# Kernel optimization log

Measured on AMD Instinct MI355X. Metric: run time of the kernel, lower is better.

The kernel has to match this reference:

```python
import jax, jax.numpy as jnp
import numpy as np

D = 1024      # n_embd
F = 1024      # moe_inter_dim (ffn_hidden_size)
E = 8         # moe_num_experts
K = 2         # moe_top_k
B, T = 2, 2048


def setup_inputs() -> dict:
    key = jax.random.key(0)
    ks = jax.random.split(key, 7)
    std = 0.02
    x = jax.random.normal(ks[0], (B, T, D), dtype=jnp.float32)
    router_w = jax.random.normal(ks[1], (D, E), dtype=jnp.float32) * std
    w1 = jax.random.normal(ks[2], (E, D, F), dtype=jnp.float32) * std  # expert up proj
    w2 = jax.random.normal(ks[3], (E, F, D), dtype=jnp.float32) * std  # expert down proj
    shared_gate_up = jax.random.normal(ks[4], (D, 2 * F), dtype=jnp.float32) * std
    shared_down = jax.random.normal(ks[5], (F, D), dtype=jnp.float32) * std
    shared_gate_w = jax.random.normal(ks[6], (D, 1), dtype=jnp.float32) * std
    return {"x": x, "router_w": router_w, "w1": w1, "w2": w2,
            "shared_gate_up": shared_gate_up, "shared_down": shared_down,
            "shared_gate_w": shared_gate_w}


def _moe_forward(x, router_w, w1, w2, shared_gate_up, shared_down, shared_gate_w):
    b, t, d = x.shape
    xf = x.reshape(-1, d)                                   # [N, D]
    n = xf.shape[0]

    # --- router: softmax over experts, top-k scores used directly as combine weights ---
    logits = xf @ router_w                                  # [N, E]
    probs = jax.nn.softmax(logits, axis=-1)
    topw, topi = jax.lax.top_k(probs, K)                    # [N, K]
    combine = jnp.zeros((n, E), dtype=probs.dtype).at[
        jnp.arange(n)[:, None], topi].add(topw)             # [N, E] sparse combine weights

    # --- expert MLP: h = silu(x @ w1_e) @ w2_e, combined with routing weights ---
    h = jax.nn.silu(jnp.einsum('nd,edf->nef', xf, w1))      # [N, E, F]
    ye = jnp.einsum('nef,efd->ned', h, w2)                  # [N, E, D]
    routed = jnp.einsum('ne,ned->nd', combine, ye)          # [N, D]

    # --- shared expert SwiGLU, gated by sigmoid(x @ shared_gate_w) ---
    gu = xf @ shared_gate_up                                # [N, 2F]
    gate, up = gu[:, :F], gu[:, F:]
    shared = (jax.nn.silu(gate) * up) @ shared_down         # [N, D]
    shared = jax.nn.sigmoid(xf @ shared_gate_w) * shared

    return (routed + shared).reshape(b, t, d)


def reference(x, router_w, w1, w2, shared_gate_up, shared_down, shared_gate_w):
    return _moe_forward(x, router_w, w1, w2, shared_gate_up, shared_down, shared_gate_w)
```

## Files before the change

kernel.cpp:

```cpp
#include <hip/hip_runtime.h>
#include <math.h>

typedef __bf16 bf16_t;
typedef __bf16 bf16x8 __attribute__((ext_vector_type(8)));
typedef __bf16 bf16x4 __attribute__((ext_vector_type(4)));
typedef float f32x4 __attribute__((ext_vector_type(4)));

#define N_TOK 4096
#define DMODEL 1024
#define FFN 1024
#define NEXP 8
#define HIST_BLK 16

#define BM 128
#define BN 128
#define BK 32
#define LDK 32

__device__ __forceinline__ void gload16(const bf16_t* g, bf16_t* l) {
  __builtin_amdgcn_global_load_lds((const __attribute__((address_space(1))) void*)g,
                                   (__attribute__((address_space(3))) void*)l, 16, 0, 0);
}

__global__ void transpose_all_kernel(const float* __restrict__ w1, const float* __restrict__ w2,
                                     const float* __restrict__ sgu, const float* __restrict__ sdw,
                                     bf16_t* __restrict__ w1t, bf16_t* __restrict__ w2t,
                                     bf16_t* __restrict__ sgut, bf16_t* __restrict__ sdt) {
  __shared__ float tile[32][33];
  const int z = blockIdx.z;
  const float* in;
  bf16_t* out;
  int C = 1024;
  bool remap = false;
  if (z < 8) {
    in = w1 + (size_t)z * 1048576; out = w1t + (size_t)z * 1048576;
  } else if (z < 16) {
    in = w2 + (size_t)(z - 8) * 1048576; out = w2t + (size_t)(z - 8) * 1048576;
  } else if (z == 16) {
    in = sgu; out = sgut; C = 2048; remap = true;
  } else {
    in = sdw; out = sdt;
  }
  const int R = 1024;
  const int c0 = blockIdx.x * 32, r0 = blockIdx.y * 32;
  if (c0 >= C) return;
  const int tx = threadIdx.x, ty = threadIdx.y;
#pragma unroll
  for (int i = 0; i < 32; i += 8)
    tile[ty + i][tx] = in[(size_t)(r0 + ty + i) * C + (c0 + tx)];
  __syncthreads();
#pragma unroll
  for (int i = 0; i < 32; i += 8) {
    int c = c0 + ty + i;
    int oc = remap ? ((c < FFN) ? 2 * c : 2 * (c - FFN) + 1) : c;
    out[(size_t)oc * R + (r0 + tx)] = (bf16_t)tile[tx][ty + i];
  }
}

__global__ void router_kernel(const float* __restrict__ x, const float* __restrict__ rw,
                              const float* __restrict__ gw, bf16_t* __restrict__ xb,
                              int* __restrict__ topi, float* __restrict__ topw,
                              float* __restrict__ sig) {
  const int t = blockIdx.x;
  const int lane = threadIdx.x;
  const float* xr = x + (size_t)t * DMODEL;
  bf16_t* xbr = xb + (size_t)t * DMODEL;
  float acc[NEXP] = {0.f, 0.f, 0.f, 0.f, 0.f, 0.f, 0.f, 0.f};
  float accg = 0.f;
#pragma unroll
  for (int i = 0; i < 4; i++) {
    const int d = i * 256 + lane * 4;
    float4 xv = *reinterpret_cast<const float4*>(xr + d);
    bf16x4 o;
    o[0] = (bf16_t)xv.x; o[1] = (bf16_t)xv.y; o[2] = (bf16_t)xv.z; o[3] = (bf16_t)xv.w;
    *reinterpret_cast<bf16x4*>(xbr + d) = o;
    const float xs[4] = {xv.x, xv.y, xv.z, xv.w};
#pragma unroll
    for (int j = 0; j < 4; j++) {
      const float4* r = reinterpret_cast<const float4*>(rw + (size_t)(d + j) * NEXP);
      float4 r0 = r[0], r1 = r[1];
      float xj = xs[j];
      acc[0] += xj * r0.x; acc[1] += xj * r0.y; acc[2] += xj * r0.z; acc[3] += xj * r0.w;
      acc[4] += xj * r1.x; acc[5] += xj * r1.y; acc[6] += xj * r1.z; acc[7] += xj * r1.w;
      accg += xj * gw[d + j];
    }
  }
#pragma unroll
  for (int e = 0; e < NEXP; e++)
    for (int s = 32; s > 0; s >>= 1) acc[e] += __shfl_down(acc[e], s, 64);
  for (int s = 32; s > 0; s >>= 1) accg += __shfl_down(accg, s, 64);
  if (lane == 0) {
    float mx = acc[0];
#pragma unroll
    for (int e = 1; e < NEXP; e++) mx = fmaxf(mx, acc[e]);
    float p[NEXP], sum = 0.f;
#pragma unroll
    for (int e = 0; e < NEXP; e++) { p[e] = __expf(acc[e] - mx); sum += p[e]; }
    int i1 = 0;
#pragma unroll
    for (int e = 1; e < NEXP; e++) if (acc[e] > acc[i1]) i1 = e;
    int i2 = (i1 == 0) ? 1 : 0;
#pragma unroll
    for (int e = 0; e < NEXP; e++) if (e != i1 && acc[e] > acc[i2]) i2 = e;
    float inv = 1.f / sum;
    topi[2 * t] = i1;     topw[2 * t] = p[i1] * inv;
    topi[2 * t + 1] = i2; topw[2 * t + 1] = p[i2] * inv;
    sig[t] = 1.f / (1.f + __expf(-accg));
  }
}

__global__ void hist_kernel(const int* __restrict__ topi, int* __restrict__ block_counts) {
  __shared__ int h[NEXP];
  const int tid = threadIdx.x;
  if (tid < NEXP) h[tid] = 0;
  __syncthreads();
  const int t = blockIdx.x * 256 + tid;
  atomicAdd(&h[topi[2 * t]], 1);
  atomicAdd(&h[topi[2 * t + 1]], 1);
  __syncthreads();
  if (tid < NEXP) block_counts[blockIdx.x * NEXP + tid] = h[tid];
}

__global__ void gather_kernel(const int* __restrict__ topi, const float* __restrict__ topw,
                              const int* __restrict__ block_counts, int* __restrict__ slot_tok,
                              float* __restrict__ slot_w, int* __restrict__ slot_of,
                              int* __restrict__ offsets, int* __restrict__ counts) {
  __shared__ int cur[NEXP];
  const int tid = threadIdx.x;
  if (tid < NEXP) {
    int off = 0;
    for (int f = 0; f < tid; f++)
      for (int b = 0; b < HIST_BLK; b++) off += block_counts[b * NEXP + f];
    int bb = off;
    for (int b = 0; b < (int)blockIdx.x; b++) bb += block_counts[b * NEXP + tid];
    cur[tid] = bb;
    if (blockIdx.x == 0) {
      offsets[tid] = off;
      int tot = 0;
      for (int b = 0; b < HIST_BLK; b++) tot += block_counts[b * NEXP + tid];
      counts[tid] = tot;
    }
  }
  __syncthreads();
  const int t = blockIdx.x * 256 + tid;
#pragma unroll
  for (int j = 0; j < 2; j++) {
    int e = topi[2 * t + j];
    int s = atomicAdd(&cur[e], 1);
    slot_tok[s] = t;
    slot_w[s] = topw[2 * t + j];
    slot_of[2 * t + j] = s;
  }
}

__global__ void combine_kernel(const bf16_t* __restrict__ Y, const int* __restrict__ slot_of,
                               float* __restrict__ out) {
  int i = blockIdx.x * blockDim.x + threadIdx.x;
  int t = i >> 7;
  int d = (i & 127) << 3;
  int s0 = slot_of[2 * t], s1 = slot_of[2 * t + 1];
  bf16x8 a = *reinterpret_cast<const bf16x8*>(Y + (size_t)s0 * DMODEL + d);
  bf16x8 b = *reinterpret_cast<const bf16x8*>(Y + (size_t)s1 * DMODEL + d);
  float* o = out + (size_t)t * DMODEL + d;
  float4 o0 = *reinterpret_cast<float4*>(o);
  float4 o1 = *reinterpret_cast<float4*>(o + 4);
  o0.x += (float)a[0] + (float)b[0]; o0.y += (float)a[1] + (float)b[1];
  o0.z += (float)a[2] + (float)b[2]; o0.w += (float)a[3] + (float)b[3];
  o1.x += (float)a[4] + (float)b[4]; o1.y += (float)a[5] + (float)b[5];
  o1.z += (float)a[6] + (float)b[6]; o1.w += (float)a[7] + (float)b[7];
  *reinterpret_cast<float4*>(o) = o0;
  *reinterpret_cast<float4*>(o + 4) = o1;
}

template <int MODE>
__global__ __launch_bounds__(256) void gemm_kernel(
    const bf16_t* __restrict__ A, const bf16_t* __restrict__ B, void* __restrict__ Cout,
    int N, const int* __restrict__ offsets, const int* __restrict__ counts,
    const int* __restrict__ slot_tok, const float* __restrict__ slot_w,
    const float* __restrict__ sig) {
  __shared__ bf16_t lds_a[BM * LDK];
  __shared__ bf16_t lds_b[BN * LDK];

  const int e = blockIdx.z;
  int m0, mEnd;
  const bf16_t* Bp = B;
  if (MODE == 1 || MODE == 2) {
    const int off = offsets[e], cnt = counts[e];
    m0 = off + (int)blockIdx.y * BM;
    mEnd = off + cnt;
    if (m0 >= mEnd) return;
    Bp += (size_t)e * FFN * DMODEL;
  } else {
    m0 = blockIdx.y * BM;
    mEnd = N_TOK;
  }
  const int n0 = blockIdx.x * BN;

  const int tid = threadIdx.x;
  const int lane = tid & 63;
  const int wave = tid >> 6;
  const int wm = (wave >> 1) * 64;
  const int wn = (wave & 1) * 64;
  const int qd = lane >> 4;
  const int lm = lane & 15;

  const int srow = wave * 16 + (lane >> 2);
  const int chunk = (lane & 3) ^ ((lane >> 3) & 3);
  const bf16_t* pa[2];
  const bf16_t* pb[2];
#pragma unroll
  for (int h = 0; h < 2; h++) {
    int s = m0 + srow + h * 64;
    int g;
    if (MODE == 1) g = slot_tok[(s < mEnd) ? s : (mEnd - 1)];
    else if (MODE == 2) g = (s < mEnd) ? s : (mEnd - 1);
    else g = s;
    pa[h] = A + (size_t)g * 1024 + chunk * 8;
    pb[h] = Bp + (size_t)(n0 + srow + h * 64) * 1024 + chunk * 8;
  }
  bf16_t* la[2] = {&lds_a[(wave * 16) * LDK], &lds_a[(64 + wave * 16) * LDK]};
  bf16_t* lb[2] = {&lds_b[(wave * 16) * LDK], &lds_b[(64 + wave * 16) * LDK]};

  f32x4 acc[4][4] = {};

  const int rkey = (lm >> 1) & 3;

  for (int k0 = 0; k0 < 1024; k0 += BK) {
    __syncthreads();
#pragma unroll
    for (int h = 0; h < 2; h++) {
      gload16(pa[h] + k0, la[h]);
      gload16(pb[h] + k0, lb[h]);
    }
    __syncthreads();
    bf16x8 af[4], bfr[4];
#pragma unroll
    for (int i = 0; i < 4; i++)
      af[i] = *reinterpret_cast<const bf16x8*>(
          &lds_a[(wm + i * 16 + lm) * LDK + ((qd ^ rkey) * 8)]);
#pragma unroll
    for (int j = 0; j < 4; j++)
      bfr[j] = *reinterpret_cast<const bf16x8*>(
          &lds_b[(wn + j * 16 + lm) * LDK + ((qd ^ rkey) * 8)]);
#pragma unroll
    for (int i = 0; i < 4; i++)
#pragma unroll
      for (int j = 0; j < 4; j++)
        acc[i][j] = __builtin_amdgcn_mfma_f32_16x16x32_bf16(af[i], bfr[j], acc[i][j], 0, 0, 0);
  }

#pragma unroll
  for (int i = 0; i < 4; i++) {
#pragma unroll
    for (int r = 0; r < 4; r++) {
      const int gm = m0 + wm + i * 16 + qd * 4 + r;
      const bool mOk = (MODE == 0 || MODE == 3) || (gm < mEnd);
      const float wgt = (MODE == 2 && mOk) ? slot_w[gm] : 0.f;
#pragma unroll
      for (int j = 0; j < 4; j++) {
        const int col = n0 + wn + j * 16 + lm;
        float v = acc[i][j][r];
        if (MODE == 0) {
          float u = __shfl_xor(v, 1, 64);
          if ((lane & 1) == 0) {
            float sv = v / (1.f + __expf(-v)) * u;
            ((bf16_t*)Cout)[(size_t)gm * FFN + (col >> 1)] = (bf16_t)sv;
          }
        } else if (MODE == 1) {
          if (mOk) ((bf16_t*)Cout)[(size_t)gm * FFN + col] = (bf16_t)(v / (1.f + __expf(-v)));
        } else if (MODE == 2) {
          if (mOk) ((bf16_t*)Cout)[(size_t)gm * DMODEL + col] = (bf16_t)(wgt * v);
        } else {
          ((float*)Cout)[(size_t)gm * DMODEL + col] = sig[gm] * v;
        }
      }
    }
  }
}

extern "C" void kernel_launch(void* const* d_in, const int* in_sizes, int n_in, void* d_out,
                              int out_size, void* d_ws, size_t ws_size, hipStream_t stream) {
  const float* x = (const float*)d_in[0];
  const float* rw = (const float*)d_in[1];
  const float* w1 = (const float*)d_in[2];
  const float* w2 = (const float*)d_in[3];
  const float* sgu = (const float*)d_in[4];
  const float* sdw = (const float*)d_in[5];
  const float* gw = (const float*)d_in[6];
  float* out = (float*)d_out;

  char* ws = (char*)d_ws;
  size_t off = 0;
  auto alloc = [&](size_t bytes) -> void* {
    void* p = ws + off;
    off += (bytes + 255) & ~(size_t)255;
    return p;
  };
  bf16_t* xb = (bf16_t*)alloc((size_t)N_TOK * DMODEL * 2);
  bf16_t* w1t = (bf16_t*)alloc((size_t)NEXP * DMODEL * FFN * 2);
  bf16_t* w2t = (bf16_t*)alloc((size_t)NEXP * DMODEL * FFN * 2);
  bf16_t* sgut = (bf16_t*)alloc((size_t)2 * FFN * DMODEL * 2);
  bf16_t* sdt = (bf16_t*)alloc((size_t)DMODEL * FFN * 2);
  bf16_t* S = (bf16_t*)alloc((size_t)N_TOK * FFN * 2);
  bf16_t* H = (bf16_t*)alloc((size_t)N_TOK * 2 * FFN * 2);
  bf16_t* Y = (bf16_t*)alloc((size_t)N_TOK * 2 * DMODEL * 2);
  int* topi = (int*)alloc(N_TOK * 2 * 4);
  float* topw = (float*)alloc(N_TOK * 2 * 4);
  float* sig = (float*)alloc(N_TOK * 4);
  int* slot_tok = (int*)alloc(N_TOK * 2 * 4);
  float* slot_w = (float*)alloc(N_TOK * 2 * 4);
  int* slot_of = (int*)alloc(N_TOK * 2 * 4);
  int* block_counts = (int*)alloc(HIST_BLK * NEXP * 4);
  int* counts = (int*)alloc(NEXP * 4);
  int* offsets = (int*)alloc(NEXP * 4);

  transpose_all_kernel<<<dim3(64, 32, 18), dim3(32, 8), 0, stream>>>(w1, w2, sgu, sdw, w1t, w2t,
                                                                     sgut, sdt);
  router_kernel<<<N_TOK, 64, 0, stream>>>(x, rw, gw, xb, topi, topw, sig);
  hist_kernel<<<HIST_BLK, 256, 0, stream>>>(topi, block_counts);
  gather_kernel<<<HIST_BLK, 256, 0, stream>>>(topi, topw, block_counts, slot_tok, slot_w,
                                              slot_of, offsets, counts);

  gemm_kernel<0><<<dim3(2 * FFN / BN, N_TOK / BM, 1), 256, 0, stream>>>(
      xb, sgut, S, 2 * FFN, nullptr, nullptr, nullptr, nullptr, nullptr);
  gemm_kernel<1><<<dim3(FFN / BN, N_TOK / BM, NEXP), 256, 0, stream>>>(
      xb, w1t, H, FFN, offsets, counts, slot_tok, nullptr, nullptr);
  gemm_kernel<2><<<dim3(DMODEL / BN, N_TOK / BM, NEXP), 256, 0, stream>>>(
      H, w2t, Y, DMODEL, offsets, counts, slot_tok, slot_w, nullptr);
  gemm_kernel<3><<<dim3(DMODEL / BN, N_TOK / BM, 1), 256, 0, stream>>>(
      S, sdt, out, DMODEL, nullptr, nullptr, nullptr, nullptr, sig);
  combine_kernel<<<N_TOK * DMODEL / 8 / 256, 256, 0, stream>>>(Y, slot_of, out);
}
```

Measured before the change: 290.2 us.

## Merge shared and routed expert GEMMs into two combined launches

Merges the shared-expert up-projection with the routed expert up-projection into one launch, and the shared down-projection with the routed down-projection into another, using blockIdx.z to select the workload. This cuts launches from four to two and lets the shared and routed blocks fill the GPU together instead of each GEMM leaving a tail of idle compute units. In exchange, every block does extra runtime branching on the workload type, and register pressure may rise because both epilogues are compiled into one kernel.

```diff
diff --git a/kernel.cpp b/kernel.cpp
--- a/kernel.cpp
+++ b/kernel.cpp
@@ -172,29 +172,36 @@
   *reinterpret_cast<float4*>(o + 4) = o1;
 }
 
-template <int MODE>
+template <int PHASE>
 __global__ __launch_bounds__(256) void gemm_kernel(
-    const bf16_t* __restrict__ A, const bf16_t* __restrict__ B, void* __restrict__ Cout,
-    int N, const int* __restrict__ offsets, const int* __restrict__ counts,
+    const bf16_t* __restrict__ As, const bf16_t* __restrict__ Bs, void* __restrict__ Cs,
+    const bf16_t* __restrict__ Ae, const bf16_t* __restrict__ Be, void* __restrict__ Ce,
+    const int* __restrict__ offsets, const int* __restrict__ counts,
     const int* __restrict__ slot_tok, const float* __restrict__ slot_w,
     const float* __restrict__ sig) {
   __shared__ bf16_t lds_a[BM * LDK];
   __shared__ bf16_t lds_b[BN * LDK];
 
-  const int e = blockIdx.z;
-  int m0, mEnd;
-  const bf16_t* Bp = B;
-  if (MODE == 1 || MODE == 2) {
+  const int z = blockIdx.z;
+  const bool sh = (PHASE == 0) ? (z < 2) : (z == 0);
+  int m0, mEnd, n0;
+  const bf16_t* Ap;
+  const bf16_t* Bp;
+  void* Cp;
+  if (sh) {
+    n0 = (PHASE == 0) ? ((z * 8 + blockIdx.x) * BN) : (blockIdx.x * BN);
+    m0 = blockIdx.y * BM;
+    mEnd = N_TOK;
+    Ap = As; Bp = Bs; Cp = Cs;
+  } else {
+    const int e = (PHASE == 0) ? (z - 2) : (z - 1);
     const int off = offsets[e], cnt = counts[e];
     m0 = off + (int)blockIdx.y * BM;
     mEnd = off + cnt;
     if (m0 >= mEnd) return;
-    Bp += (size_t)e * FFN * DMODEL;
-  } else {
-    m0 = blockIdx.y * BM;
-    mEnd = N_TOK;
-  }
-  const int n0 = blockIdx.x * BN;
+    n0 = blockIdx.x * BN;
+    Ap = Ae; Bp = Be + (size_t)e * FFN * DMODEL; Cp = Ce;
+  }
 
   const int tid = threadIdx.x;
   const int lane = tid & 63;
@@ -211,11 +218,9 @@
 #pragma unroll
   for (int h = 0; h < 2; h++) {
     int s = m0 + srow + h * 64;
-    int g;
-    if (MODE == 1) g = slot_tok[(s < mEnd) ? s : (mEnd - 1)];
-    else if (MODE == 2) g = (s < mEnd) ? s : (mEnd - 1);
-    else g = s;
-    pa[h] = A + (size_t)g * 1024 + chunk * 8;
+    int sc = (s < mEnd) ? s : (mEnd - 1);
+    int g = (PHASE == 0 && !sh) ? slot_tok[sc] : sc;
+    pa[h] = Ap + (size_t)g * 1024 + chunk * 8;
     pb[h] = Bp + (size_t)(n0 + srow + h * 64) * 1024 + chunk * 8;
   }
   bf16_t* la[2] = {&lds_a[(wave * 16) * LDK], &lds_a[(64 + wave * 16) * LDK]};
@@ -254,24 +259,28 @@
 #pragma unroll
     for (int r = 0; r < 4; r++) {
       const int gm = m0 + wm + i * 16 + qd * 4 + r;
-      const bool mOk = (MODE == 0 || MODE == 3) || (gm < mEnd);
-      const float wgt = (MODE == 2 && mOk) ? slot_w[gm] : 0.f;
+      const bool mOk = sh || (gm < mEnd);
+      const float wgt = (PHASE == 1 && !sh && mOk) ? slot_w[gm] : 0.f;
 #pragma unroll
       for (int j = 0; j < 4; j++) {
         const int col = n0 + wn + j * 16 + lm;
         float v = acc[i][j][r];
-        if (MODE == 0) {
-          float u = __shfl_xor(v, 1, 64);
-          if ((lane & 1) == 0) {
-            float sv = v / (1.f + __expf(-v)) * u;
-            ((bf16_t*)Cout)[(size_t)gm * FFN + (col >> 1)] = (bf16_t)sv;
+        if (PHASE == 0) {
+          if (sh) {
+            float u = __shfl_xor(v, 1, 64);
+            if ((lane & 1) == 0) {
+              float sv = v / (1.f + __expf(-v)) * u;
+              ((bf16_t*)Cp)[(size_t)gm * FFN + (col >> 1)] = (bf16_t)sv;
+            }
+          } else {
+            if (mOk) ((bf16_t*)Cp)[(size_t)gm * FFN + col] = (bf16_t)(v / (1.f + __expf(-v)));
           }
-        } else if (MODE == 1) {
-          if (mOk) ((bf16_t*)Cout)[(size_t)gm * FFN + col] = (bf16_t)(v / (1.f + __expf(-v)));
-        } else if (MODE == 2) {
-          if (mOk) ((bf16_t*)Cout)[(size_t)gm * DMODEL + col] = (bf16_t)(wgt * v);
         } else {
-          ((float*)Cout)[(size_t)gm * DMODEL + col] = sig[gm] * v;
+          if (sh) {
+            ((float*)Cp)[(size_t)gm * DMODEL + col] = sig[gm] * v;
+          } else {
+            if (mOk) ((bf16_t*)Cp)[(size_t)gm * DMODEL + col] = (bf16_t)(wgt * v);
+          }
         }
       }
     }
@@ -321,13 +330,9 @@
   gather_kernel<<<HIST_BLK, 256, 0, stream>>>(topi, topw, block_counts, slot_tok, slot_w,
                                               slot_of, offsets, counts);
 
-  gemm_kernel<0><<<dim3(2 * FFN / BN, N_TOK / BM, 1), 256, 0, stream>>>(
-      xb, sgut, S, 2 * FFN, nullptr, nullptr, nullptr, nullptr, nullptr);
-  gemm_kernel<1><<<dim3(FFN / BN, N_TOK / BM, NEXP), 256, 0, stream>>>(
-      xb, w1t, H, FFN, offsets, counts, slot_tok, nullptr, nullptr);
-  gemm_kernel<2><<<dim3(DMODEL / BN, N_TOK / BM, NEXP), 256, 0, stream>>>(
-      H, w2t, Y, DMODEL, offsets, counts, slot_tok, slot_w, nullptr);
-  gemm_kernel<3><<<dim3(DMODEL / BN, N_TOK / BM, 1), 256, 0, stream>>>(
-      S, sdt, out, DMODEL, nullptr, nullptr, nullptr, nullptr, sig);
+  gemm_kernel<0><<<dim3(8, N_TOK / BM, 2 + NEXP), 256, 0, stream>>>(
+      xb, sgut, S, xb, w1t, H, offsets, counts, slot_tok, nullptr, nullptr);
+  gemm_kernel<1><<<dim3(DMODEL / BN, N_TOK / BM, 1 + NEXP), 256, 0, stream>>>(
+      S, sdt, out, H, w2t, Y, offsets, counts, slot_tok, slot_w, sig);
   combine_kernel<<<N_TOK * DMODEL / 8 / 256, 256, 0, stream>>>(Y, slot_of, out);
 }
```

Result: slower. 300.1 us (+3.4%).

## Double-buffer LDS tiles with BK=64 to overlap global loads and MFMA

Applied to the files above, without the earlier changes.

Doubles the K tile to 64 and adds a two-stage LDS ping-pong buffer, so the async global-to-LDS loads for the next tile are issued before the MFMAs on the current tile, replacing the load-sync-compute-sync pattern. The XOR swizzle is adjusted to 8 chunks per row and the staging layout changes so each wave loads 8 rows per pass. This is meant to hide global memory latency and halve barrier count. In exchange LDS usage rises to 64 KB per block, which may reduce occupancy.

```diff
diff --git a/kernel.cpp b/kernel.cpp
--- a/kernel.cpp
+++ b/kernel.cpp
@@ -14,8 +14,8 @@
 
 #define BM 128
 #define BN 128
-#define BK 32
-#define LDK 32
+#define BK 64
+#define NT (1024 / BK)
 
 __device__ __forceinline__ void gload16(const bf16_t* g, bf16_t* l) {
   __builtin_amdgcn_global_load_lds((const __attribute__((address_space(1))) void*)g,
@@ -178,8 +178,7 @@
     int N, const int* __restrict__ offsets, const int* __restrict__ counts,
     const int* __restrict__ slot_tok, const float* __restrict__ slot_w,
     const float* __restrict__ sig) {
-  __shared__ bf16_t lds_a[BM * LDK];
-  __shared__ bf16_t lds_b[BN * LDK];
+  __shared__ bf16_t lds[2][(BM + BN) * BK];
 
   const int e = blockIdx.z;
   int m0, mEnd;
@@ -204,49 +203,58 @@
   const int qd = lane >> 4;
   const int lm = lane & 15;
 
-  const int srow = wave * 16 + (lane >> 2);
-  const int chunk = (lane & 3) ^ ((lane >> 3) & 3);
-  const bf16_t* pa[2];
-  const bf16_t* pb[2];
-#pragma unroll
-  for (int h = 0; h < 2; h++) {
-    int s = m0 + srow + h * 64;
+  const int rsub = lane >> 3;
+  const int chunk = (lane & 7) ^ rsub;
+  const bf16_t* pa[4];
+  const bf16_t* pb[4];
+#pragma unroll
+  for (int h = 0; h < 4; h++) {
+    const int ar = h * 32 + wave * 8 + rsub;
+    int s = m0 + ar;
+    int sc = (s < mEnd) ? s : (mEnd - 1);
     int g;
-    if (MODE == 1) g = slot_tok[(s < mEnd) ? s : (mEnd - 1)];
-    else if (MODE == 2) g = (s < mEnd) ? s : (mEnd - 1);
+    if (MODE == 1) g = slot_tok[sc];
+    else if (MODE == 2) g = sc;
     else g = s;
     pa[h] = A + (size_t)g * 1024 + chunk * 8;
-    pb[h] = Bp + (size_t)(n0 + srow + h * 64) * 1024 + chunk * 8;
-  }
-  bf16_t* la[2] = {&lds_a[(wave * 16) * LDK], &lds_a[(64 + wave * 16) * LDK]};
-  bf16_t* lb[2] = {&lds_b[(wave * 16) * LDK], &lds_b[(64 + wave * 16) * LDK]};
+    pb[h] = Bp + (size_t)(n0 + ar) * 1024 + chunk * 8;
+  }
+
+  auto stage = [&](int bf, int k0) {
+#pragma unroll
+    for (int h = 0; h < 4; h++) {
+      gload16(pa[h] + k0, &lds[bf][(h * 32 + wave * 8) * BK]);
+      gload16(pb[h] + k0, &lds[bf][(BM + h * 32 + wave * 8) * BK]);
+    }
+  };
 
   f32x4 acc[4][4] = {};
-
-  const int rkey = (lm >> 1) & 3;
-
-  for (int k0 = 0; k0 < 1024; k0 += BK) {
+  const int pc0 = qd ^ (lm & 7);
+  const int pc1 = (4 + qd) ^ (lm & 7);
+
+  stage(0, 0);
+  __syncthreads();
+  for (int t = 0; t < NT; ++t) {
+    const int cur = t & 1;
+    if (t + 1 < NT) stage(cur ^ 1, (t + 1) * BK);
+#pragma unroll
+    for (int s = 0; s < 2; s++) {
+      const int pc = (s == 0) ? pc0 : pc1;
+      bf16x8 af[4], bfr[4];
+#pragma unroll
+      for (int i = 0; i < 4; i++)
+        af[i] = *reinterpret_cast<const bf16x8*>(&lds[cur][(wm + i * 16 + lm) * BK + pc * 8]);
+#pragma unroll
+      for (int j = 0; j < 4; j++)
+        bfr[j] =
+            *reinterpret_cast<const bf16x8*>(&lds[cur][(BM + wn + j * 16 + lm) * BK + pc * 8]);
+#pragma unroll
+      for (int i = 0; i < 4; i++)
+#pragma unroll
+        for (int j = 0; j < 4; j++)
+          acc[i][j] = __builtin_amdgcn_mfma_f32_16x16x32_bf16(af[i], bfr[j], acc[i][j], 0, 0, 0);
+    }
     __syncthreads();
-#pragma unroll
-    for (int h = 0; h < 2; h++) {
-      gload16(pa[h] + k0, la[h]);
-      gload16(pb[h] + k0, lb[h]);
-    }
-    __syncthreads();
-    bf16x8 af[4], bfr[4];
-#pragma unroll
-    for (int i = 0; i < 4; i++)
-      af[i] = *reinterpret_cast<const bf16x8*>(
-          &lds_a[(wm + i * 16 + lm) * LDK + ((qd ^ rkey) * 8)]);
-#pragma unroll
-    for (int j = 0; j < 4; j++)
-      bfr[j] = *reinterpret_cast<const bf16x8*>(
-          &lds_b[(wn + j * 16 + lm) * LDK + ((qd ^ rkey) * 8)]);
-#pragma unroll
-    for (int i = 0; i < 4; i++)
-#pragma unroll
-      for (int j = 0; j < 4; j++)
-        acc[i][j] = __builtin_amdgcn_mfma_f32_16x16x32_bf16(af[i], bfr[j], acc[i][j], 0, 0, 0);
   }
 
 #pragma unroll
```

After: 289.8 us. No clear change (-0.1%).

## Add 4-stage LDS prefetch pipeline and remap block indices in GEMM

Applied to the files above, without the earlier changes.

Replaces the single-buffered load-sync-compute loop with a four-buffer software pipeline. Each stage issues global_load_lds for tile k+3 while computing tile k, using explicit vmcnt waits and s_barriers. It also remaps the flat block index so consecutive blocks walk the M dimension first, which should improve reuse of weight tiles in L2. This aims to hide global memory latency behind MFMA work, at the cost of 4x the LDS footprint and hardcoded wait counts that assume four loads per stage and 32 K-steps.

```diff
diff --git a/kernel.cpp b/kernel.cpp
--- a/kernel.cpp
+++ b/kernel.cpp
@@ -15,7 +15,7 @@
 #define BM 128
 #define BN 128
 #define BK 32
-#define LDK 32
+#define NT 32
 
 __device__ __forceinline__ void gload16(const bf16_t* g, bf16_t* l) {
   __builtin_amdgcn_global_load_lds((const __attribute__((address_space(1))) void*)g,
@@ -178,23 +178,29 @@
     int N, const int* __restrict__ offsets, const int* __restrict__ counts,
     const int* __restrict__ slot_tok, const float* __restrict__ slot_w,
     const float* __restrict__ sig) {
-  __shared__ bf16_t lds_a[BM * LDK];
-  __shared__ bf16_t lds_b[BN * LDK];
+  __shared__ bf16_t ldsb0[(BM + BN) * BK];
+  __shared__ bf16_t ldsb1[(BM + BN) * BK];
+  __shared__ bf16_t ldsb2[(BM + BN) * BK];
+  __shared__ bf16_t ldsb3[(BM + BN) * BK];
+
+  const int f = (int)blockIdx.y * (int)gridDim.x + (int)blockIdx.x;
+  const int nby = f & 31;
+  const int nbx = f >> 5;
 
   const int e = blockIdx.z;
   int m0, mEnd;
   const bf16_t* Bp = B;
   if (MODE == 1 || MODE == 2) {
     const int off = offsets[e], cnt = counts[e];
-    m0 = off + (int)blockIdx.y * BM;
+    m0 = off + nby * BM;
     mEnd = off + cnt;
     if (m0 >= mEnd) return;
     Bp += (size_t)e * FFN * DMODEL;
   } else {
-    m0 = blockIdx.y * BM;
+    m0 = nby * BM;
     mEnd = N_TOK;
   }
-  const int n0 = blockIdx.x * BN;
+  const int n0 = nbx * BN;
 
   const int tid = threadIdx.x;
   const int lane = tid & 63;
@@ -206,48 +212,90 @@
 
   const int srow = wave * 16 + (lane >> 2);
   const int chunk = (lane & 3) ^ ((lane >> 3) & 3);
-  const bf16_t* pa[2];
-  const bf16_t* pb[2];
-#pragma unroll
-  for (int h = 0; h < 2; h++) {
-    int s = m0 + srow + h * 64;
-    int g;
-    if (MODE == 1) g = slot_tok[(s < mEnd) ? s : (mEnd - 1)];
-    else if (MODE == 2) g = (s < mEnd) ? s : (mEnd - 1);
-    else g = s;
-    pa[h] = A + (size_t)g * 1024 + chunk * 8;
-    pb[h] = Bp + (size_t)(n0 + srow + h * 64) * 1024 + chunk * 8;
-  }
-  bf16_t* la[2] = {&lds_a[(wave * 16) * LDK], &lds_a[(64 + wave * 16) * LDK]};
-  bf16_t* lb[2] = {&lds_b[(wave * 16) * LDK], &lds_b[(64 + wave * 16) * LDK]};
+  int s0r = m0 + srow, s1r = m0 + srow + 64;
+  int sc0 = (s0r < mEnd) ? s0r : (mEnd - 1);
+  int sc1 = (s1r < mEnd) ? s1r : (mEnd - 1);
+  int g0, g1;
+  if (MODE == 1) { g0 = slot_tok[sc0]; g1 = slot_tok[sc1]; }
+  else if (MODE == 2) { g0 = sc0; g1 = sc1; }
+  else { g0 = s0r; g1 = s1r; }
+  const bf16_t* pa0 = A + (size_t)g0 * 1024 + chunk * 8;
+  const bf16_t* pa1 = A + (size_t)g1 * 1024 + chunk * 8;
+  const bf16_t* pb0 = Bp + (size_t)(n0 + srow) * 1024 + chunk * 8;
+  const bf16_t* pb1 = Bp + (size_t)(n0 + srow + 64) * 1024 + chunk * 8;
 
   f32x4 acc[4][4] = {};
-
-  const int rkey = (lm >> 1) & 3;
-
-  for (int k0 = 0; k0 < 1024; k0 += BK) {
-    __syncthreads();
-#pragma unroll
-    for (int h = 0; h < 2; h++) {
-      gload16(pa[h] + k0, la[h]);
-      gload16(pb[h] + k0, lb[h]);
-    }
-    __syncthreads();
-    bf16x8 af[4], bfr[4];
-#pragma unroll
-    for (int i = 0; i < 4; i++)
-      af[i] = *reinterpret_cast<const bf16x8*>(
-          &lds_a[(wm + i * 16 + lm) * LDK + ((qd ^ rkey) * 8)]);
-#pragma unroll
-    for (int j = 0; j < 4; j++)
-      bfr[j] = *reinterpret_cast<const bf16x8*>(
-          &lds_b[(wn + j * 16 + lm) * LDK + ((qd ^ rkey) * 8)]);
-#pragma unroll
-    for (int i = 0; i < 4; i++)
-#pragma unroll
-      for (int j = 0; j < 4; j++)
-        acc[i][j] = __builtin_amdgcn_mfma_f32_16x16x32_bf16(af[i], bfr[j], acc[i][j], 0, 0, 0);
-  }
+  const int pcr = qd ^ ((lm >> 1) & 3);
+
+#define SBAR0 __builtin_amdgcn_sched_barrier(0)
+#define STAGE(LDSB, T)                                          \
+  do {                                                          \
+    const int k0s = (T) * BK;                                   \
+    gload16(pa0 + k0s, &LDSB[(wave * 16) * BK]);                \
+    gload16(pa1 + k0s, &LDSB[(64 + wave * 16) * BK]);           \
+    gload16(pb0 + k0s, &LDSB[(BM + wave * 16) * BK]);           \
+    gload16(pb1 + k0s, &LDSB[(BM + 64 + wave * 16) * BK]);      \
+  } while (0)
+
+#define COMPUTE(LDSB)                                                        \
+  do {                                                                       \
+    bf16x8 af[4], bfr[4];                                                    \
+    _Pragma("unroll") for (int i = 0; i < 4; i++)                            \
+        af[i] = *reinterpret_cast<const bf16x8*>(                            \
+            &LDSB[(wm + i * 16 + lm) * BK + pcr * 8]);                       \
+    _Pragma("unroll") for (int j = 0; j < 4; j++)                            \
+        bfr[j] = *reinterpret_cast<const bf16x8*>(                           \
+            &LDSB[(BM + wn + j * 16 + lm) * BK + pcr * 8]);                  \
+    _Pragma("unroll") for (int i = 0; i < 4; i++)                            \
+        _Pragma("unroll") for (int j = 0; j < 4; j++)                        \
+            acc[i][j] = __builtin_amdgcn_mfma_f32_16x16x32_bf16(             \
+                af[i], bfr[j], acc[i][j], 0, 0, 0);                          \
+  } while (0)
+
+#define ITER_S(T, CBUF, PBUF, WAIT)       \
+  do {                                    \
+    STAGE(PBUF, (T) + 3);                 \
+    SBAR0;                                \
+    asm volatile(WAIT ::: "memory");      \
+    __builtin_amdgcn_s_barrier();         \
+    SBAR0;                                \
+    COMPUTE(CBUF);                        \
+    SBAR0;                                \
+    __builtin_amdgcn_s_barrier();         \
+    SBAR0;                                \
+  } while (0)
+#define ITER_N(CBUF, WAIT)                \
+  do {                                    \
+    SBAR0;                                \
+    asm volatile(WAIT ::: "memory");      \
+    __builtin_amdgcn_s_barrier();         \
+    SBAR0;                                \
+    COMPUTE(CBUF);                        \
+    SBAR0;                                \
+    __builtin_amdgcn_s_barrier();         \
+    SBAR0;                                \
+  } while (0)
+
+  STAGE(ldsb0, 0);
+  STAGE(ldsb1, 1);
+  STAGE(ldsb2, 2);
+
+  for (int tt = 0; tt < 28; tt += 4) {
+    ITER_S(tt + 0, ldsb0, ldsb3, "s_waitcnt vmcnt(12)");
+    ITER_S(tt + 1, ldsb1, ldsb0, "s_waitcnt vmcnt(12)");
+    ITER_S(tt + 2, ldsb2, ldsb1, "s_waitcnt vmcnt(12)");
+    ITER_S(tt + 3, ldsb3, ldsb2, "s_waitcnt vmcnt(12)");
+  }
+  ITER_S(28, ldsb0, ldsb3, "s_waitcnt vmcnt(12)");
+  ITER_N(ldsb1, "s_waitcnt vmcnt(8)");
+  ITER_N(ldsb2, "s_waitcnt vmcnt(4)");
+  ITER_N(ldsb3, "s_waitcnt vmcnt(0)");
+
+#undef ITER_N
+#undef ITER_S
+#undef COMPUTE
+#undef STAGE
+#undef SBAR0
 
 #pragma unroll
   for (int i = 0; i < 4; i++) {
```

Measured after the change: 386.1 us. 1.33x slower.
